# Optimization experiments

Measured on AMD Instinct MI355X. Metric: run time of the kernel, lower is better.

The kernel has to match this reference:

```python
import jax, jax.numpy as jnp
import numpy as np

F = 26          # field_size
D = 16          # embed_dim
B = 16384       # batch
VOCABS = [1000] * F
OFFSETS = np.concatenate([[0], np.cumsum(VOCABS)[:-1]]).astype(np.int32)
IU, JU = np.triu_indices(F, k=1)   # 325 pairs (i<j)
P = IU.shape[0]
BN_EPS = 1e-3   # Keras BatchNormalization default epsilon


def setup_inputs() -> dict:
    key = jax.random.key(0)
    ks = jax.random.split(key, 8)
    s = 0.05  # keras 'random_normal' initializer stddev
    return {
        "x": jax.random.randint(ks[0], (B, F), 0, 1000, dtype=jnp.int32),
        "emb_table": jax.random.normal(ks[1], (sum(VOCABS) + 1, D), jnp.float32) * s,
        "se_w1": jax.random.normal(ks[2], (F, F // 2), jnp.float32) * s,
        "se_w2": jax.random.normal(ks[3], (F // 2, F), jnp.float32) * s,
        "bl_w": jax.random.normal(ks[4], (P, D, D), jnp.float32) * s,
        "w1": jax.random.normal(ks[5], (F * (F - 1) * D, 64), jnp.float32) * s,
        "b1": jnp.zeros((64,), jnp.float32),
        "g1": jnp.ones((64,), jnp.float32),
        "be1": jnp.zeros((64,), jnp.float32),
        "m1": jnp.zeros((64,), jnp.float32),
        "v1": jnp.ones((64,), jnp.float32),
        "w2": jax.random.normal(ks[6], (64, 32), jnp.float32) * s,
        "b2": jnp.zeros((32,), jnp.float32),
        "g2": jnp.ones((32,), jnp.float32),
        "be2": jnp.zeros((32,), jnp.float32),
        "m2": jnp.zeros((32,), jnp.float32),
        "v2": jnp.ones((32,), jnp.float32),
        "w3": jax.random.normal(ks[7], (32, 1), jnp.float32) * s,
        "b3": jnp.zeros((1,), jnp.float32),
    }


def _bilinear(v, bl_w):
    # v: [B, F, D]; shared W stack over the 325 ordered pairs (i<j)
    # tmp[p] = (v_i @ W_p) * v_j  -> [B, P, D]
    return jnp.einsum('bpd,pde->bpe', v[:, IU], bl_w) * v[:, JU]


def _bn(h, g, b, m, v):
    return g * (h - m) * jax.lax.rsqrt(v + BN_EPS) + b


def reference(x, emb_table, se_w1, se_w2, bl_w,
              w1, b1, g1, be1, m1, v1,
              w2, b2, g2, be2, m2, v2,
              w3, b3):
    ids = x + jnp.asarray(OFFSETS)
    e = emb_table[ids]                         # [B, F, D]
    # SE layer: mean-pool over embed dim, two ReLU dense layers, rescale
    z = e.mean(axis=-1)                        # [B, F]
    A = jax.nn.relu(jax.nn.relu(z @ se_w1) @ se_w2)
    se = e * A[..., None]                      # [B, F, D]
    # Bilinear interaction (same weights for both calls)
    p = _bilinear(e, bl_w).reshape(e.shape[0], -1)     # [B, P*D]
    se_p = _bilinear(se, bl_w).reshape(e.shape[0], -1)
    h = jnp.concatenate([p, se_p], axis=-1)    # [B, F*(F-1)*D]
    # MLP with inference-mode BatchNorm; dropout=0 is a no-op
    h = jax.nn.relu(_bn(h @ w1 + b1, g1, be1, m1, v1))
    h = jax.nn.relu(_bn(h @ w2 + b2, g2, be2, m2, v2))
    return jax.nn.sigmoid(h @ w3 + b3)         # [B, 1]
```

## Files before the change

### kernel.cpp

```cpp
#include <hip/hip_runtime.h>
#include <cstdint>
#include <cstddef>


#define F_FIELDS 26
#define P_PAIRS 325
#define PAD_PAIRS 336
#define BATCH 16384
#define BN_EPS 1e-3f

typedef short bf16x8 __attribute__((ext_vector_type(8)));
typedef float f32x4 __attribute__((ext_vector_type(4)));

struct PairTab { unsigned char iu[PAD_PAIRS]; unsigned char ju[PAD_PAIRS]; };
static constexpr PairTab make_pairs() {
    PairTab t{};
    int p = 0;
    for (int a = 0; a < F_FIELDS; ++a)
        for (int b = a + 1; b < F_FIELDS; ++b) { t.iu[p] = (unsigned char)a; t.ju[p] = (unsigned char)b; ++p; }
    for (; p < PAD_PAIRS; ++p) { t.iu[p] = 0; t.ju[p] = 0; }
    return t;
}
__constant__ PairTab PT = make_pairs();

__device__ __forceinline__ unsigned short bf16u(float v) {
    unsigned u = __float_as_uint(v);
    unsigned r = (u + 0x7fffu + ((u >> 16) & 1u)) >> 16;
    return (unsigned short)r;
}
__device__ __forceinline__ unsigned pk_bf16(float lo, float hi) {
    return (unsigned)bf16u(lo) | ((unsigned)bf16u(hi) << 16);
}
__device__ __forceinline__ float bflo(unsigned d) { return __uint_as_float(d << 16); }
__device__ __forceinline__ float bfhi(unsigned d) { return __uint_as_float(d & 0xffff0000u); }
__device__ __forceinline__ unsigned pk_trunc(float u, float cu) {
    return __builtin_amdgcn_perm(__float_as_uint(cu), __float_as_uint(u), 0x07060302u);
}

__global__ __launch_bounds__(256) void k_wprep(const float* __restrict__ w1,
        const float* __restrict__ blw, unsigned short* __restrict__ w1catL,
        unsigned short* __restrict__ wcatL) {
    const int p = blockIdx.x;
    const int tid = threadIdx.x;
    if (p >= P_PAIRS) {
        int4 z = make_int4(0, 0, 0, 0);
        *(int4*)(w1catL + (size_t)p * 2048 + tid * 8) = z;
        if (tid < 64) *(int4*)(wcatL + (size_t)p * 512 + tid * 8) = z;
        return;
    }
    __shared__ float wu[1024], wv[1024], wb[256];
    ((float4*)wu)[tid] = ((const float4*)(w1 + (size_t)p * 1024))[tid];
    ((float4*)wv)[tid] = ((const float4*)(w1 + 332800 + (size_t)p * 1024))[tid];
    if (tid < 64) ((float4*)wb)[tid] = ((const float4*)(blw + (size_t)p * 256))[tid];
    __syncthreads();
    {
        int nt = tid >> 6, lane = tid & 63, ln = lane & 15, q = lane >> 4;
        int o = nt * 16 + ln;
        unsigned short outv[8];
        #pragma unroll
        for (int j = 0; j < 8; ++j) {
            int k = q * 8 + j, d = k >> 1, su = k & 1;
            outv[j] = bf16u(su ? wv[d * 64 + o] : wu[d * 64 + o]);
        }
        *(int4*)(w1catL + (size_t)p * 2048 + tid * 8) = *(const int4*)outv;
    }
    if (tid < 64) {
        int ln = tid & 15, q = tid >> 4;
        unsigned short outv[8];
        #pragma unroll
        for (int j = 0; j < 8; ++j) {
            int din = q * 8 + j;
            outv[j] = (din < 16) ? bf16u(wb[din * 16 + ln]) : (unsigned short)0;
        }
        *(int4*)(wcatL + (size_t)p * 512 + tid * 8) = *(const int4*)outv;
    }
}

union __align__(16) SMem {
    struct {
        unsigned short eS[32 * 424];
        float aS[F_FIELDS * 32];
    } a;
    struct {
        unsigned ysh[8 * 4 * 64 * 4];
        float h1s[32 * 65];
        float h2s[32 * 36];
    } b;
};

__global__ __launch_bounds__(512, 4) void k_main(const int* __restrict__ x,
        const float* __restrict__ emb, const float* __restrict__ sw1,
        const float* __restrict__ sw2, const unsigned short* __restrict__ w1catL,
        const unsigned short* __restrict__ wcatL,
        const float* __restrict__ b1, const float* __restrict__ g1,
        const float* __restrict__ be1, const float* __restrict__ m1,
        const float* __restrict__ v1,
        const float* __restrict__ w2, const float* __restrict__ b2,
        const float* __restrict__ g2, const float* __restrict__ be2,
        const float* __restrict__ m2, const float* __restrict__ v2,
        const float* __restrict__ w3, const float* __restrict__ b3,
        float* __restrict__ out) {
    __shared__ SMem sm;
    __shared__ float z_s[32][F_FIELDS];
    __shared__ float sw1_s[F_FIELDS * 13];
    __shared__ float sw2_s[13 * F_FIELDS];
    const int tid = threadIdx.x;
    const int b0 = blockIdx.x * 32;
    unsigned short* eS = sm.a.eS;
    float* aS = sm.a.aS;

    for (int i = tid; i < F_FIELDS * 13; i += 512) { sw1_s[i] = sw1[i]; sw2_s[i] = sw2[i]; }
    for (int idx = tid; idx < 32 * F_FIELDS; idx += 512) {
        int r = idx / F_FIELDS, f = idx - r * F_FIELDS;
        int id = x[(b0 + r) * F_FIELDS + f] + f * 1000;
        const float4* src = (const float4*)(emb + (size_t)id * 16);
        float4 v0 = src[0], v1l = src[1], v2l = src[2], v3l = src[3];
        int4 o0, o1;
        o0.x = (int)pk_bf16(v0.x, v0.y);  o0.y = (int)pk_bf16(v0.z, v0.w);
        o0.z = (int)pk_bf16(v1l.x, v1l.y); o0.w = (int)pk_bf16(v1l.z, v1l.w);
        o1.x = (int)pk_bf16(v2l.x, v2l.y); o1.y = (int)pk_bf16(v2l.z, v2l.w);
        o1.z = (int)pk_bf16(v3l.x, v3l.y); o1.w = (int)pk_bf16(v3l.z, v3l.w);
        *(int4*)(eS + r * 424 + f * 16) = o0;
        *(int4*)(eS + r * 424 + f * 16 + 8) = o1;
        float s = v0.x + v0.y + v0.z + v0.w + v1l.x + v1l.y + v1l.z + v1l.w
                + v2l.x + v2l.y + v2l.z + v2l.w + v3l.x + v3l.y + v3l.z + v3l.w;
        z_s[r][f] = s * (1.0f / 16.0f);
    }
    __syncthreads();
    if (tid < 32) {
        float s1[13];
        #pragma unroll
        for (int o = 0; o < 13; ++o) {
            float acc0 = 0.f;
            #pragma unroll
            for (int f = 0; f < F_FIELDS; ++f) acc0 = fmaf(z_s[tid][f], sw1_s[f * 13 + o], acc0);
            s1[o] = fmaxf(acc0, 0.0f);
        }
        #pragma unroll
        for (int f = 0; f < F_FIELDS; ++f) {
            float acc0 = 0.f;
            #pragma unroll
            for (int o = 0; o < 13; ++o) acc0 = fmaf(s1[o], sw2_s[o * F_FIELDS + f], acc0);
            aS[f * 32 + tid] = fmaxf(acc0, 0.0f);
        }
    }
    __syncthreads();

    const int w    = tid >> 6;
    const int lane = tid & 63;
    const int ln   = lane & 15;
    const int q    = lane >> 4;
    const int p0 = w * 42, p1 = p0 + 42;

    f32x4 acc[2][4];
    #pragma unroll
    for (int a = 0; a < 2; ++a)
        #pragma unroll
        for (int b = 0; b < 4; ++b) acc[a][b] = (f32x4){0.f, 0.f, 0.f, 0.f};
    const f32x4 zero4 = {0.f, 0.f, 0.f, 0.f};

    int iu_c = PT.iu[p0];
    bf16x8 eiB[2];
    float ai[2];
    #pragma unroll
    for (int mt = 0; mt < 2; ++mt) {
        eiB[mt] = __builtin_bit_cast(bf16x8,
            *(const int4*)(eS + (mt * 16 + ln) * 424 + iu_c * 16 + (q & 1) * 8));
        ai[mt] = aS[iu_c * 32 + mt * 16 + ln];
    }
    bf16x8 wa_c = __builtin_bit_cast(bf16x8, *(const int4*)(wcatL + (size_t)p0 * 512 + lane * 8));
    bf16x8 wb_c[4];
    #pragma unroll
    for (int nt = 0; nt < 4; ++nt)
        wb_c[nt] = __builtin_bit_cast(bf16x8, *(const int4*)(w1catL + (size_t)p0 * 2048 + nt * 512 + lane * 8));
    f32x4 tc[2];
    #pragma unroll
    for (int mt = 0; mt < 2; ++mt)
        tc[mt] = __builtin_amdgcn_mfma_f32_16x16x32_bf16(wa_c, eiB[mt], zero4, 0, 0, 0);

    #pragma unroll 2
    for (int p = p0; p < p1; ++p) {
        const int pn = (p + 1 < p1) ? (p + 1) : p;
        bf16x8 wa_n = __builtin_bit_cast(bf16x8, *(const int4*)(wcatL + (size_t)pn * 512 + lane * 8));
        bf16x8 wb_n[4];
        #pragma unroll
        for (int nt = 0; nt < 4; ++nt)
            wb_n[nt] = __builtin_bit_cast(bf16x8, *(const int4*)(w1catL + (size_t)pn * 2048 + nt * 512 + lane * 8));

        const int ju = PT.ju[p];
        uint2 ejv[2];
        float cv[2];
        #pragma unroll
        for (int mt = 0; mt < 2; ++mt) {
            ejv[mt] = *(const uint2*)(eS + (mt * 16 + ln) * 424 + ju * 16 + q * 4);
            cv[mt]  = ai[mt] * aS[ju * 32 + mt * 16 + ln];
        }
        const int iu_n = PT.iu[pn];
        if (iu_n != iu_c) {
            iu_c = iu_n;
            #pragma unroll
            for (int mt = 0; mt < 2; ++mt) {
                eiB[mt] = __builtin_bit_cast(bf16x8,
                    *(const int4*)(eS + (mt * 16 + ln) * 424 + iu_c * 16 + (q & 1) * 8));
                ai[mt] = aS[iu_c * 32 + mt * 16 + ln];
            }
        }
        f32x4 tn[2];
        #pragma unroll
        for (int mt = 0; mt < 2; ++mt)
            tn[mt] = __builtin_amdgcn_mfma_f32_16x16x32_bf16(wa_n, eiB[mt], zero4, 0, 0, 0);

        #pragma unroll
        for (int mt = 0; mt < 2; ++mt) {
            f32x4 t = tc[mt];
            float e0 = bflo(ejv[mt].x), e1 = bfhi(ejv[mt].x);
            float e2 = bflo(ejv[mt].y), e3 = bfhi(ejv[mt].y);
            float c  = cv[mt];
            float u0 = t[0] * e0, u1 = t[1] * e1, u2 = t[2] * e2, u3 = t[3] * e3;
            int4 af;
            af.x = (int)pk_trunc(u0, c * u0);
            af.y = (int)pk_trunc(u1, c * u1);
            af.z = (int)pk_trunc(u2, c * u2);
            af.w = (int)pk_trunc(u3, c * u3);
            bf16x8 A = __builtin_bit_cast(bf16x8, af);
            #pragma unroll
            for (int nt = 0; nt < 4; ++nt)
                acc[mt][nt] = __builtin_amdgcn_mfma_f32_16x16x32_bf16(A, wb_c[nt], acc[mt][nt], 0, 0, 0);
        }
        tc[0] = tn[0]; tc[1] = tn[1];
        wa_c = wa_n;
        #pragma unroll
        for (int nt = 0; nt < 4; ++nt) wb_c[nt] = wb_n[nt];
    }

    __syncthreads();
    unsigned* ysh = sm.b.ysh;
    float* h1s = sm.b.h1s;
    float* h2s = sm.b.h2s;
    #pragma unroll
    for (int mt = 0; mt < 2; ++mt)
        #pragma unroll
        for (int nh = 0; nh < 2; ++nh) {
            int nt0 = nh * 2, nt1 = nh * 2 + 1;
            int4 v;
            v.x = (int)pk_bf16(acc[mt][nt0][0], acc[mt][nt0][1]);
            v.y = (int)pk_bf16(acc[mt][nt0][2], acc[mt][nt0][3]);
            v.z = (int)pk_bf16(acc[mt][nt1][0], acc[mt][nt1][1]);
            v.w = (int)pk_bf16(acc[mt][nt1][2], acc[mt][nt1][3]);
            *(int4*)(ysh + ((w * 4 + mt * 2 + nh) * 64 + lane) * 4) = v;
        }
    __syncthreads();

    if (tid < 256) {
        const int s = tid >> 6, lane2 = tid & 63, ln2 = lane2 & 15, q2 = lane2 >> 4;
        const int mt = s >> 1, nh = s & 1;
        const int c0 = nh * 32 + ln2, c1 = c0 + 16;
        const float sc0 = g1[c0] * rsqrtf(v1[c0] + BN_EPS);
        const float of0 = be1[c0] + sc0 * (b1[c0] - m1[c0]);
        const float sc1 = g1[c1] * rsqrtf(v1[c1] + BN_EPS);
        const float of1 = be1[c1] + sc1 * (b1[c1] - m1[c1]);
        float s8[8];
        #pragma unroll
        for (int i = 0; i < 8; ++i) s8[i] = 0.f;
        #pragma unroll
        for (int wv = 0; wv < 8; ++wv) {
            int4 v = *(const int4*)(ysh + ((wv * 4 + s) * 64 + lane2) * 4);
            s8[0] += bflo((unsigned)v.x); s8[1] += bfhi((unsigned)v.x);
            s8[2] += bflo((unsigned)v.y); s8[3] += bfhi((unsigned)v.y);
            s8[4] += bflo((unsigned)v.z); s8[5] += bfhi((unsigned)v.z);
            s8[6] += bflo((unsigned)v.w); s8[7] += bfhi((unsigned)v.w);
        }
        const int row0 = mt * 16 + q2 * 4;
        #pragma unroll
        for (int r = 0; r < 4; ++r) {
            h1s[(row0 + r) * 65 + c0] = fmaxf(s8[r] * sc0 + of0, 0.f);
            h1s[(row0 + r) * 65 + c1] = fmaxf(s8[4 + r] * sc1 + of1, 0.f);
        }
    }
    __syncthreads();

    {
        const int row = tid >> 4, gg = tid & 15;
        const int o0 = gg * 2, o1 = o0 + 1;
        float a0 = 0.f, a1 = 0.f;
        #pragma unroll 8
        for (int k = 0; k < 64; ++k) {
            float hk = h1s[row * 65 + k];
            float2 wv = *(const float2*)(w2 + k * 32 + o0);
            a0 = fmaf(hk, wv.x, a0);
            a1 = fmaf(hk, wv.y, a1);
        }
        float val0 = g2[o0] * (a0 + b2[o0] - m2[o0]) * rsqrtf(v2[o0] + BN_EPS) + be2[o0];
        float val1 = g2[o1] * (a1 + b2[o1] - m2[o1]) * rsqrtf(v2[o1] + BN_EPS) + be2[o1];
        h2s[row * 36 + o0] = fmaxf(val0, 0.f);
        h2s[row * 36 + o1] = fmaxf(val1, 0.f);
    }
    __syncthreads();
    if (tid < 32) {
        float sacc = b3[0];
        #pragma unroll
        for (int k = 0; k < 32; ++k) sacc = fmaf(h2s[tid * 36 + k], w3[k], sacc);
        out[b0 + tid] = 1.0f / (1.0f + expf(-sacc));
    }
}

extern "C" void kernel_launch(void* const* d_in, const int* in_sizes, int n_in,
                              void* d_out, int out_size, void* d_ws, size_t ws_size,
                              hipStream_t stream) {
    const int*   x   = (const int*)d_in[0];
    const float* emb = (const float*)d_in[1];
    const float* sw1 = (const float*)d_in[2];
    const float* sw2 = (const float*)d_in[3];
    const float* blw = (const float*)d_in[4];
    const float* w1  = (const float*)d_in[5];
    const float* b1  = (const float*)d_in[6];
    const float* g1  = (const float*)d_in[7];
    const float* be1 = (const float*)d_in[8];
    const float* m1  = (const float*)d_in[9];
    const float* v1  = (const float*)d_in[10];
    const float* w2  = (const float*)d_in[11];
    const float* b2  = (const float*)d_in[12];
    const float* g2  = (const float*)d_in[13];
    const float* be2 = (const float*)d_in[14];
    const float* m2  = (const float*)d_in[15];
    const float* v2  = (const float*)d_in[16];
    const float* w3  = (const float*)d_in[17];
    const float* b3  = (const float*)d_in[18];
    float* out = (float*)d_out;

    char* ws = (char*)d_ws;
    unsigned short* w1catL = (unsigned short*)ws;
    unsigned short* wcatL  = (unsigned short*)(ws + 1376256);

    hipLaunchKernelGGL(k_wprep, dim3(PAD_PAIRS), dim3(256), 0, stream, w1, blw, w1catL, wcatL);
    hipLaunchKernelGGL(k_main,  dim3(512), dim3(512), 0, stream,
                       x, emb, sw1, sw2, w1catL, wcatL,
                       b1, g1, be1, m1, v1, w2, b2, g2, be2, m2, v2, w3, b3, out);
}
```

Measured before the change: 147.0 us.

## Double batch rows per block to amortize weight loads across more MFMA tiles

Each block now handles 64 batch rows instead of 32, so every streamed W1 and bilinear weight fragment feeds four M-tiles instead of two. Total global weight traffic per batch row drops, and the grid halves to 256 blocks. The bilinear MFMA for the next pair is moved after the accumulate loop instead of being software-pipelined ahead of it. In exchange, register and LDS use per block grow, and launch bounds drop to 2 blocks per CU, which lowers occupancy and leaves fewer blocks than before to fill the CUs.

Result: faster. 136.6 us (-7.1%).

```diff
diff --git a/kernel.cpp b/kernel.cpp
--- a/kernel.cpp
+++ b/kernel.cpp
@@ -8,6 +8,7 @@
 #define PAD_PAIRS 336
 #define BATCH 16384
 #define BN_EPS 1e-3f
+#define ROWS 64
 
 typedef short bf16x8 __attribute__((ext_vector_type(8)));
 typedef float f32x4 __attribute__((ext_vector_type(4)));
@@ -78,17 +79,17 @@
 
 union __align__(16) SMem {
     struct {
-        unsigned short eS[32 * 424];
-        float aS[F_FIELDS * 32];
+        unsigned short eS[ROWS * 424];
+        float aS[F_FIELDS * ROWS];
     } a;
     struct {
-        unsigned ysh[8 * 4 * 64 * 4];
-        float h1s[32 * 65];
-        float h2s[32 * 36];
+        unsigned ysh[8 * 8 * 64 * 4];
+        float h1s[ROWS * 65];
+        float h2s[ROWS * 36];
     } b;
 };
 
-__global__ __launch_bounds__(512, 4) void k_main(const int* __restrict__ x,
+__global__ __launch_bounds__(512, 2) void k_main(const int* __restrict__ x,
         const float* __restrict__ emb, const float* __restrict__ sw1,
         const float* __restrict__ sw2, const unsigned short* __restrict__ w1catL,
         const unsigned short* __restrict__ wcatL,
@@ -101,16 +102,16 @@
         const float* __restrict__ w3, const float* __restrict__ b3,
         float* __restrict__ out) {
     __shared__ SMem sm;
-    __shared__ float z_s[32][F_FIELDS];
+    __shared__ float z_s[ROWS][F_FIELDS];
     __shared__ float sw1_s[F_FIELDS * 13];
     __shared__ float sw2_s[13 * F_FIELDS];
     const int tid = threadIdx.x;
-    const int b0 = blockIdx.x * 32;
+    const int b0 = blockIdx.x * ROWS;
     unsigned short* eS = sm.a.eS;
     float* aS = sm.a.aS;
 
     for (int i = tid; i < F_FIELDS * 13; i += 512) { sw1_s[i] = sw1[i]; sw2_s[i] = sw2[i]; }
-    for (int idx = tid; idx < 32 * F_FIELDS; idx += 512) {
+    for (int idx = tid; idx < ROWS * F_FIELDS; idx += 512) {
         int r = idx / F_FIELDS, f = idx - r * F_FIELDS;
         int id = x[(b0 + r) * F_FIELDS + f] + f * 1000;
         const float4* src = (const float4*)(emb + (size_t)id * 16);
@@ -127,7 +128,7 @@
         z_s[r][f] = s * (1.0f / 16.0f);
     }
     __syncthreads();
-    if (tid < 32) {
+    if (tid < ROWS) {
         float s1[13];
         #pragma unroll
         for (int o = 0; o < 13; ++o) {
@@ -141,7 +142,7 @@
             float acc0 = 0.f;
             #pragma unroll
             for (int o = 0; o < 13; ++o) acc0 = fmaf(s1[o], sw2_s[o * F_FIELDS + f], acc0);
-            aS[f * 32 + tid] = fmaxf(acc0, 0.0f);
+            aS[f * ROWS + tid] = fmaxf(acc0, 0.0f);
         }
     }
     __syncthreads();
@@ -152,30 +153,30 @@
     const int q    = lane >> 4;
     const int p0 = w * 42, p1 = p0 + 42;
 
-    f32x4 acc[2][4];
-    #pragma unroll
-    for (int a = 0; a < 2; ++a)
+    f32x4 acc[4][4];
+    #pragma unroll
+    for (int a = 0; a < 4; ++a)
         #pragma unroll
         for (int b = 0; b < 4; ++b) acc[a][b] = (f32x4){0.f, 0.f, 0.f, 0.f};
     const f32x4 zero4 = {0.f, 0.f, 0.f, 0.f};
 
     int iu_c = PT.iu[p0];
-    bf16x8 eiB[2];
-    float ai[2];
-    #pragma unroll
-    for (int mt = 0; mt < 2; ++mt) {
+    bf16x8 eiB[4];
+    float ai[4];
+    #pragma unroll
+    for (int mt = 0; mt < 4; ++mt) {
         eiB[mt] = __builtin_bit_cast(bf16x8,
             *(const int4*)(eS + (mt * 16 + ln) * 424 + iu_c * 16 + (q & 1) * 8));
-        ai[mt] = aS[iu_c * 32 + mt * 16 + ln];
+        ai[mt] = aS[iu_c * ROWS + mt * 16 + ln];
     }
     bf16x8 wa_c = __builtin_bit_cast(bf16x8, *(const int4*)(wcatL + (size_t)p0 * 512 + lane * 8));
     bf16x8 wb_c[4];
     #pragma unroll
     for (int nt = 0; nt < 4; ++nt)
         wb_c[nt] = __builtin_bit_cast(bf16x8, *(const int4*)(w1catL + (size_t)p0 * 2048 + nt * 512 + lane * 8));
-    f32x4 tc[2];
-    #pragma unroll
-    for (int mt = 0; mt < 2; ++mt)
+    f32x4 tc[4];
+    #pragma unroll
+    for (int mt = 0; mt < 4; ++mt)
         tc[mt] = __builtin_amdgcn_mfma_f32_16x16x32_bf16(wa_c, eiB[mt], zero4, 0, 0, 0);
 
     #pragma unroll 2
@@ -188,30 +189,26 @@
             wb_n[nt] = __builtin_bit_cast(bf16x8, *(const int4*)(w1catL + (size_t)pn * 2048 + nt * 512 + lane * 8));
 
         const int ju = PT.ju[p];
-        uint2 ejv[2];
-        float cv[2];
-        #pragma unroll
-        for (int mt = 0; mt < 2; ++mt) {
+        uint2 ejv[4];
+        float cv[4];
+        #pragma unroll
+        for (int mt = 0; mt < 4; ++mt) {
             ejv[mt] = *(const uint2*)(eS + (mt * 16 + ln) * 424 + ju * 16 + q * 4);
-            cv[mt]  = ai[mt] * aS[ju * 32 + mt * 16 + ln];
+            cv[mt]  = ai[mt] * aS[ju * ROWS + mt * 16 + ln];
         }
         const int iu_n = PT.iu[pn];
         if (iu_n != iu_c) {
             iu_c = iu_n;
             #pragma unroll
-            for (int mt = 0; mt < 2; ++mt) {
+            for (int mt = 0; mt < 4; ++mt) {
                 eiB[mt] = __builtin_bit_cast(bf16x8,
                     *(const int4*)(eS + (mt * 16 + ln) * 424 + iu_c * 16 + (q & 1) * 8));
-                ai[mt] = aS[iu_c * 32 + mt * 16 + ln];
+                ai[mt] = aS[iu_c * ROWS + mt * 16 + ln];
             }
         }
-        f32x4 tn[2];
-        #pragma unroll
-        for (int mt = 0; mt < 2; ++mt)
-            tn[mt] = __builtin_amdgcn_mfma_f32_16x16x32_bf16(wa_n, eiB[mt], zero4, 0, 0, 0);
-
-        #pragma unroll
-        for (int mt = 0; mt < 2; ++mt) {
+
+        #pragma unroll
+        for (int mt = 0; mt < 4; ++mt) {
             f32x4 t = tc[mt];
             float e0 = bflo(ejv[mt].x), e1 = bfhi(ejv[mt].x);
             float e2 = bflo(ejv[mt].y), e3 = bfhi(ejv[mt].y);
@@ -227,7 +224,9 @@
             for (int nt = 0; nt < 4; ++nt)
                 acc[mt][nt] = __builtin_amdgcn_mfma_f32_16x16x32_bf16(A, wb_c[nt], acc[mt][nt], 0, 0, 0);
         }
-        tc[0] = tn[0]; tc[1] = tn[1];
+        #pragma unroll
+        for (int mt = 0; mt < 4; ++mt)
+            tc[mt] = __builtin_amdgcn_mfma_f32_16x16x32_bf16(wa_n, eiB[mt], zero4, 0, 0, 0);
         wa_c = wa_n;
         #pragma unroll
         for (int nt = 0; nt < 4; ++nt) wb_c[nt] = wb_n[nt];
@@ -238,7 +237,7 @@
     float* h1s = sm.b.h1s;
     float* h2s = sm.b.h2s;
     #pragma unroll
-    for (int mt = 0; mt < 2; ++mt)
+    for (int mt = 0; mt < 4; ++mt)
         #pragma unroll
         for (int nh = 0; nh < 2; ++nh) {
             int nt0 = nh * 2, nt1 = nh * 2 + 1;
@@ -247,11 +246,11 @@
             v.y = (int)pk_bf16(acc[mt][nt0][2], acc[mt][nt0][3]);
             v.z = (int)pk_bf16(acc[mt][nt1][0], acc[mt][nt1][1]);
             v.w = (int)pk_bf16(acc[mt][nt1][2], acc[mt][nt1][3]);
-            *(int4*)(ysh + ((w * 4 + mt * 2 + nh) * 64 + lane) * 4) = v;
-        }
-    __syncthreads();
-
-    if (tid < 256) {
+            *(int4*)(ysh + ((w * 8 + mt * 2 + nh) * 64 + lane) * 4) = v;
+        }
+    __syncthreads();
+
+    {
         const int s = tid >> 6, lane2 = tid & 63, ln2 = lane2 & 15, q2 = lane2 >> 4;
         const int mt = s >> 1, nh = s & 1;
         const int c0 = nh * 32 + ln2, c1 = c0 + 16;
@@ -264,7 +263,7 @@
         for (int i = 0; i < 8; ++i) s8[i] = 0.f;
         #pragma unroll
         for (int wv = 0; wv < 8; ++wv) {
-            int4 v = *(const int4*)(ysh + ((wv * 4 + s) * 64 + lane2) * 4);
+            int4 v = *(const int4*)(ysh + ((wv * 8 + s) * 64 + lane2) * 4);
             s8[0] += bflo((unsigned)v.x); s8[1] += bfhi((unsigned)v.x);
             s8[2] += bflo((unsigned)v.y); s8[3] += bfhi((unsigned)v.y);
             s8[4] += bflo((unsigned)v.z); s8[5] += bfhi((unsigned)v.z);
@@ -280,23 +279,32 @@
     __syncthreads();
 
     {
-        const int row = tid >> 4, gg = tid & 15;
-        const int o0 = gg * 2, o1 = o0 + 1;
-        float a0 = 0.f, a1 = 0.f;
+        const int row = tid >> 3, gg = tid & 7;
+        const int o0 = gg * 4;
+        float a0 = 0.f, a1 = 0.f, a2 = 0.f, a3 = 0.f;
         #pragma unroll 8
         for (int k = 0; k < 64; ++k) {
             float hk = h1s[row * 65 + k];
-            float2 wv = *(const float2*)(w2 + k * 32 + o0);
+            float4 wv = *(const float4*)(w2 + k * 32 + o0);
             a0 = fmaf(hk, wv.x, a0);
             a1 = fmaf(hk, wv.y, a1);
-        }
-        float val0 = g2[o0] * (a0 + b2[o0] - m2[o0]) * rsqrtf(v2[o0] + BN_EPS) + be2[o0];
-        float val1 = g2[o1] * (a1 + b2[o1] - m2[o1]) * rsqrtf(v2[o1] + BN_EPS) + be2[o1];
-        h2s[row * 36 + o0] = fmaxf(val0, 0.f);
-        h2s[row * 36 + o1] = fmaxf(val1, 0.f);
-    }
-    __syncthreads();
-    if (tid < 32) {
+            a2 = fmaf(hk, wv.z, a2);
+            a3 = fmaf(hk, wv.w, a3);
+        }
+        const float4 g2v  = *(const float4*)(g2 + o0);
+        const float4 b2v  = *(const float4*)(b2 + o0);
+        const float4 m2v  = *(const float4*)(m2 + o0);
+        const float4 v2v  = *(const float4*)(v2 + o0);
+        const float4 be2v = *(const float4*)(be2 + o0);
+        float4 hv;
+        hv.x = fmaxf(g2v.x * (a0 + b2v.x - m2v.x) * rsqrtf(v2v.x + BN_EPS) + be2v.x, 0.f);
+        hv.y = fmaxf(g2v.y * (a1 + b2v.y - m2v.y) * rsqrtf(v2v.y + BN_EPS) + be2v.y, 0.f);
+        hv.z = fmaxf(g2v.z * (a2 + b2v.z - m2v.z) * rsqrtf(v2v.z + BN_EPS) + be2v.z, 0.f);
+        hv.w = fmaxf(g2v.w * (a3 + b2v.w - m2v.w) * rsqrtf(v2v.w + BN_EPS) + be2v.w, 0.f);
+        *(float4*)(h2s + row * 36 + o0) = hv;
+    }
+    __syncthreads();
+    if (tid < ROWS) {
         float sacc = b3[0];
         #pragma unroll
         for (int k = 0; k < 32; ++k) sacc = fmaf(h2s[tid * 36 + k], w3[k], sacc);
@@ -333,7 +341,7 @@
     unsigned short* wcatL  = (unsigned short*)(ws + 1376256);
 
     hipLaunchKernelGGL(k_wprep, dim3(PAD_PAIRS), dim3(256), 0, stream, w1, blw, w1catL, wcatL);
-    hipLaunchKernelGGL(k_main,  dim3(512), dim3(512), 0, stream,
+    hipLaunchKernelGGL(k_main,  dim3(BATCH / ROWS), dim3(512), 0, stream,
                        x, emb, sw1, sw2, w1catL, wcatL,
                        b1, g1, be1, m1, v1, w2, b2, g2, be2, m2, v2, w3, b3, out);
 }
```
